# Kernel tuning notes

Hardware: AMD Instinct MI355X
Metric: run time of the kernel (lower is better)

Reference implementation:

```python
import jax, jax.numpy as jnp
import numpy as np

B, N, F_IN, F_OUT, E, GSD = 64, 512, 512, 512, 4, 1024
EPS = 1e-5


def _bn(z2d, gamma, beta):
    # training-mode BatchNorm1d over rows, biased variance, eps=1e-5
    mean = z2d.mean(axis=0)
    var = z2d.var(axis=0)
    return (z2d - mean) * jax.lax.rsqrt(var + EPS) * gamma + beta


def setup_inputs() -> dict:
    key = jax.random.key(0)
    ks = jax.random.split(key, 10)
    x = jax.random.normal(ks[0], (B, N, F_IN), dtype=jnp.float32)
    adj = jax.random.uniform(ks[1], (B, E, N, N), dtype=jnp.float32)
    global_state = jax.random.normal(ks[2], (B, GSD), dtype=jnp.float32)
    subgraph_sizes = jax.random.randint(ks[3], (B, 2), 0, 256, dtype=jnp.int64)
    mask = jnp.ones((B, N, 1), dtype=jnp.float32)
    # parameters
    W_gfc = jax.random.normal(ks[4], (GSD // 2, F_OUT), dtype=jnp.float32) * (1.0 / np.sqrt(GSD // 2))
    b_gfc = jnp.zeros((F_OUT,), dtype=jnp.float32)
    W_gc = jax.random.normal(ks[5], (E, F_IN + F_OUT, F_OUT), dtype=jnp.float32) * (1.0 / np.sqrt(F_IN + F_OUT))
    b_gc = jnp.zeros((F_OUT,), dtype=jnp.float32)
    gamma_n = jnp.ones((F_OUT,), dtype=jnp.float32)
    beta_n = jnp.zeros((F_OUT,), dtype=jnp.float32)
    gamma_g = jnp.ones((F_OUT,), dtype=jnp.float32)
    beta_g = jnp.zeros((F_OUT,), dtype=jnp.float32)
    return dict(x=x, adj=adj, global_state=global_state, subgraph_sizes=subgraph_sizes,
                mask=mask, W_gfc=W_gfc, b_gfc=b_gfc, W_gc=W_gc, b_gc=b_gc,
                gamma_n=gamma_n, beta_n=beta_n, gamma_g=gamma_g, beta_g=beta_g)


def reference(x, adj, global_state, subgraph_sizes, mask,
              W_gfc, b_gfc, W_gc, b_gc, gamma_n, beta_n, gamma_g, beta_g):
    b, n, _ = x.shape
    o = W_gfc.shape[1]
    # global FC on the two halves of the global state
    gs = global_state.reshape(b, 2, -1)                 # [B,2,GSD/2]
    gt = jnp.einsum('bkg,go->bko', gs, W_gfc) + b_gfc   # [B,2,O]
    # data-dependent broadcast of global features into node slices (vectorized)
    n1 = subgraph_sizes[:, 0]
    n2 = subgraph_sizes[:, 1]
    idx = jnp.arange(n)[None, :]
    sel0 = (idx < n1[:, None]).astype(x.dtype)                                  # [B,N]
    sel1 = ((idx >= n1[:, None]) & (idx < (n1 + n2)[:, None])).astype(x.dtype)  # [B,N]
    bg = sel0[..., None] * gt[:, 0, None, :] + sel1[..., None] * gt[:, 1, None, :]  # [B,N,O]
    x_concat = jnp.concatenate([x, bg], axis=-1)        # [B,N,F_IN+O]
    # multi-relational graph convolution: sum_e adj_e @ (x W_e) + bias
    support = jnp.einsum('bnf,efo->beno', x_concat, W_gc)       # [B,E,N,O]
    x_out = jnp.einsum('benm,bemo->bno', adj, support) + b_gc   # [B,N,O]
    # BN + mask + relu on nodes
    x_out = _bn(x_out.reshape(-1, o), gamma_n, beta_n).reshape(b, n, o)
    x_out = jax.nn.relu(x_out * mask)
    # BN + relu on global
    g_out = _bn(gt.reshape(-1, o), gamma_g, beta_g).reshape(b, 2, o)
    g_out = jax.nn.relu(g_out).reshape(b, -1)
    return x_out, g_out
```

## Files before the change

### kernel.cpp

```cpp
#include <hip/hip_runtime.h>

#define DEVI __device__ __forceinline__

typedef __bf16 bf16x8 __attribute__((ext_vector_type(8)));
typedef float  f32x4  __attribute__((ext_vector_type(4)));
typedef unsigned short ushort8_t __attribute__((ext_vector_type(8)));

constexpr size_t XOUT_ELEMS = (size_t)64 * 512 * 512;

DEVI unsigned short f2b(float f) {
  __bf16 h = (__bf16)f;
  return __builtin_bit_cast(unsigned short, h);
}

__global__ void k_decode(const int* __restrict__ ss, int* __restrict__ ns) {
  int t = threadIdx.x;
  int odd = ss[2 * t + 1];
  unsigned long long bal = __ballot(odd == 0);
  bool is64 = (bal == 0xFFFFFFFFFFFFFFFFull);
  if (is64) {
    const long long* s64 = (const long long*)ss;
    ns[2 * t]     = (int)s64[2 * t];
    ns[2 * t + 1] = (int)s64[2 * t + 1];
  } else {
    ns[2 * t]     = ss[2 * t];
    ns[2 * t + 1] = ss[2 * t + 1];
  }
}

__global__ void k_gt(const float* __restrict__ gs, const float* __restrict__ W,
                     const float* __restrict__ bias, float* __restrict__ gt,
                     unsigned short* __restrict__ gth) {
  __shared__ float srow[4][512];
  int r0  = blockIdx.y * 4;
  int col = blockIdx.x * 256 + threadIdx.x;
  for (int i = threadIdx.x; i < 4 * 512; i += 256)
    srow[i >> 9][i & 511] = gs[(size_t)r0 * 512 + i];
  __syncthreads();
  float acc[4] = {0.f, 0.f, 0.f, 0.f};
  for (int g = 0; g < 512; ++g) {
    float w = W[(size_t)g * 512 + col];
    acc[0] += srow[0][g] * w;
    acc[1] += srow[1][g] * w;
    acc[2] += srow[2][g] * w;
    acc[3] += srow[3][g] * w;
  }
  float bb = bias[col];
  #pragma unroll
  for (int r = 0; r < 4; ++r) {
    float v = acc[r] + bb;
    gt [(size_t)(r0 + r) * 512 + col] = v;
    gth[(size_t)(r0 + r) * 512 + col] = f2b(v);
  }
}

__global__ void k_gbn(const float* __restrict__ gt, const float* __restrict__ gamma,
                      const float* __restrict__ beta, float* __restrict__ gout) {
  int col = blockIdx.x * 64 + threadIdx.x;
  float s = 0.f, q = 0.f;
  for (int r = 0; r < 128; ++r) {
    float v = gt[(size_t)r * 512 + col];
    s += v; q += v * v;
  }
  float m   = s * (1.f / 128.f);
  float var = q * (1.f / 128.f) - m * m;
  float inv = 1.f / sqrtf(var + 1e-5f);
  float g = gamma[col], b = beta[col];
  for (int r = 0; r < 128; ++r) {
    float v = (gt[(size_t)r * 512 + col] - m) * inv * g + b;
    gout[(size_t)r * 512 + col] = fmaxf(v, 0.f);
  }
}

__global__ void k_cvt(const float* __restrict__ in, unsigned short* __restrict__ out,
                      long n8) {
  long i = (long)blockIdx.x * blockDim.x + threadIdx.x;
  long stride = (long)gridDim.x * blockDim.x;
  for (; i < n8; i += stride) {
    float4 a = ((const float4*)in)[2 * i];
    float4 b = ((const float4*)in)[2 * i + 1];
    ushort8_t o;
    o[0] = f2b(a.x); o[1] = f2b(a.y); o[2] = f2b(a.z); o[3] = f2b(a.w);
    o[4] = f2b(b.x); o[5] = f2b(b.y); o[6] = f2b(b.z); o[7] = f2b(b.w);
    *(ushort8_t*)&out[i * 8] = o;
  }
}

__global__ void k_cvt_w(const float* __restrict__ W, unsigned short* __restrict__ wT) {
  __shared__ float t[32][33];
  int k0 = blockIdx.x * 32, o0 = blockIdx.y * 32, e = blockIdx.z;
  const float* Wb = W + (size_t)e * 1024 * 512;
  unsigned short* Tb = wT + (size_t)e * 512 * 1024;
  int tid = threadIdx.x;
  #pragma unroll
  for (int p = 0; p < 4; ++p) {
    int kl = p * 8 + (tid >> 5), ol = tid & 31;
    t[kl][ol] = Wb[(size_t)(k0 + kl) * 512 + o0 + ol];
  }
  __syncthreads();
  #pragma unroll
  for (int p = 0; p < 4; ++p) {
    int ol = p * 8 + (tid >> 5), kl = tid & 31;
    Tb[(size_t)(o0 + ol) * 1024 + k0 + kl] = f2b(t[kl][ol]);
  }
}

DEVI void gl_lds16(const unsigned short* g, unsigned short* l) {
  __builtin_amdgcn_global_load_lds(
      (const __attribute__((address_space(1))) void*)g,
      (__attribute__((address_space(3))) void*)l, 16, 0, 0);
}

DEVI int lds_idx(int row, int slot) {
  return row * 32 + ((slot ^ ((row >> 1) & 3)) << 3);
}

template <class FA, class FB>
DEVI void mfma_core(unsigned short* As, unsigned short* Bs, FA srcA, FB srcB,
                    int NT, f32x4 (&acc)[4][4]) {
  const int tid  = threadIdx.x;
  const int lane = tid & 63;
  const int wave = tid >> 6;
  const int wr = wave >> 1, wc = wave & 1;
  const int fr = lane & 15, fs = lane >> 4;

  const int c0 = tid,       r0 = c0 >> 2, s0 = (c0 & 3) ^ ((r0 >> 1) & 3);
  const int c1 = tid + 256, r1 = c1 >> 2, s1 = (c1 & 3) ^ ((r1 >> 1) & 3);

  int aoff[4], boff[4];
  #pragma unroll
  for (int i = 0; i < 4; ++i) {
    aoff[i] = lds_idx(wr * 64 + i * 16 + fr, fs);
    boff[i] = lds_idx(wc * 64 + i * 16 + fr, fs);
  }

  gl_lds16(srcA(r0, s0 * 8, 0), As + c0 * 8);
  gl_lds16(srcA(r1, s1 * 8, 0), As + c1 * 8);
  gl_lds16(srcB(r0, s0 * 8, 0), Bs + c0 * 8);
  gl_lds16(srcB(r1, s1 * 8, 0), Bs + c1 * 8);

  for (int kt = 0; kt < NT; ++kt) {
    __syncthreads();
    bf16x8 af[4], bf[4];
    #pragma unroll
    for (int i = 0; i < 4; ++i) af[i] = *(const bf16x8*)(As + aoff[i]);
    #pragma unroll
    for (int j = 0; j < 4; ++j) bf[j] = *(const bf16x8*)(Bs + boff[j]);
    if (kt + 1 < NT) {
      __syncthreads();
      gl_lds16(srcA(r0, s0 * 8, kt + 1), As + c0 * 8);
      gl_lds16(srcA(r1, s1 * 8, kt + 1), As + c1 * 8);
      gl_lds16(srcB(r0, s0 * 8, kt + 1), Bs + c0 * 8);
      gl_lds16(srcB(r1, s1 * 8, kt + 1), Bs + c1 * 8);
    }
    #pragma unroll
    for (int i = 0; i < 4; ++i)
      #pragma unroll
      for (int j = 0; j < 4; ++j)
        acc[i][j] = __builtin_amdgcn_mfma_f32_16x16x32_bf16(af[i], bf[j], acc[i][j], 0, 0, 0);
  }
}

__global__ __launch_bounds__(256) void k_gadd(
    const unsigned short* __restrict__ gth, const unsigned short* __restrict__ wT,
    float* __restrict__ gadd) {
  __shared__ __align__(16) unsigned short As[4096], Bs[4096];
  const int otile = blockIdx.x * 128;

  auto srcA = [=](int row, int kofs, int kt) -> const unsigned short* {
    return gth + (size_t)row * 512 + kt * 32 + kofs;
  };
  auto srcB = [=](int row, int kofs, int kt) -> const unsigned short* {
    int op = otile + row;
    int e = op >> 9, o = op & 511;
    return wT + (size_t)e * 524288 + (size_t)o * 1024 + 512 + kt * 32 + kofs;
  };

  f32x4 acc[4][4];
  #pragma unroll
  for (int i = 0; i < 4; ++i)
    #pragma unroll
    for (int j = 0; j < 4; ++j) acc[i][j] = (f32x4){0.f, 0.f, 0.f, 0.f};

  mfma_core(As, Bs, srcA, srcB, 16, acc);

  const int lane = threadIdx.x & 63, wave = threadIdx.x >> 6;
  const int wr = wave >> 1, wc = wave & 1, fr = lane & 15, fs = lane >> 4;
  #pragma unroll
  for (int i = 0; i < 4; ++i) {
    int m = wr * 64 + i * 16 + fs * 4;
    #pragma unroll
    for (int j = 0; j < 4; ++j) {
      int op = otile + wc * 64 + j * 16 + fr;
      #pragma unroll
      for (int r = 0; r < 4; ++r)
        gadd[(size_t)(m + r) * 2048 + op] = acc[i][j][r];
    }
  }
}

__global__ __launch_bounds__(256) void k_support(
    const unsigned short* __restrict__ xh, const unsigned short* __restrict__ wT,
    const float* __restrict__ gadd, const int* __restrict__ ns,
    unsigned short* __restrict__ supT, int b0, int gc) {
  __shared__ __align__(16) unsigned short As[4096], Bs[4096];
  int flat = blockIdx.x;
  const int zi = flat % gc; flat /= gc;
  const int e  = flat & 3;  flat >>= 2;
  const int otile = (flat & 3) * 128;
  const int row0  = (flat >> 2) * 128;
  const int b  = b0 + zi;
  const int n1  = ns[2 * b];
  const int n12 = n1 + ns[2 * b + 1];
  const unsigned short* xb = xh + (size_t)b * 262144;
  const unsigned short* wb = wT + (size_t)e * 524288;

  auto srcA = [=](int row, int kofs, int kt) -> const unsigned short* {
    return xb + (size_t)(row0 + row) * 512 + kt * 32 + kofs;
  };
  auto srcB = [=](int row, int kofs, int kt) -> const unsigned short* {
    return wb + (size_t)(otile + row) * 1024 + kt * 32 + kofs;
  };

  f32x4 acc[4][4];
  #pragma unroll
  for (int i = 0; i < 4; ++i)
    #pragma unroll
    for (int j = 0; j < 4; ++j) acc[i][j] = (f32x4){0.f, 0.f, 0.f, 0.f};

  mfma_core(As, Bs, srcA, srcB, 16, acc);

  const int lane = threadIdx.x & 63, wave = threadIdx.x >> 6;
  const int wr = wave >> 1, wc = wave & 1, fr = lane & 15, fs = lane >> 4;
  unsigned short* sp = supT + (size_t)(zi * 4 + e) * 262144;
  #pragma unroll
  for (int j = 0; j < 4; ++j) {
    int o = otile + wc * 64 + j * 16 + fr;
    float g0 = gadd[(size_t)(2 * b)     * 2048 + e * 512 + o];
    float g1 = gadd[(size_t)(2 * b + 1) * 2048 + e * 512 + o];
    #pragma unroll
    for (int i = 0; i < 4; ++i) {
      int m = row0 + wr * 64 + i * 16 + fs * 4;
      ushort4 h;
      #pragma unroll
      for (int r = 0; r < 4; ++r) {
        int mr = m + r;
        float add = (mr < n1) ? g0 : ((mr < n12) ? g1 : 0.f);
        ((unsigned short*)&h)[r] = f2b(acc[i][j][r] + add);
      }
      *(ushort4*)&sp[(size_t)o * 512 + m] = h;
    }
  }
}

__global__ __launch_bounds__(256) void k_xout(
    const unsigned short* __restrict__ adjh, const unsigned short* __restrict__ supT,
    const float* __restrict__ bgc, float* __restrict__ out,
    float* __restrict__ gsum, float* __restrict__ gsq, int b0, int gc) {
  __shared__ __align__(16) unsigned short As[4096], Bs[4096];
  int flat = blockIdx.x;
  const int zi = flat % gc; flat /= gc;
  const int otile = (flat & 3) * 128;
  const int row0  = (flat >> 2) * 128;
  const int b  = b0 + zi;
  const unsigned short* ab = adjh + (size_t)b * 4 * 262144;
  const unsigned short* sb = supT + (size_t)zi * 4 * 262144;

  auto srcA = [=](int row, int kofs, int kt) -> const unsigned short* {
    int k = kt * 32 + kofs;
    int e = k >> 9, m = k & 511;
    return ab + ((size_t)e * 512 + row0 + row) * 512 + m;
  };
  auto srcB = [=](int row, int kofs, int kt) -> const unsigned short* {
    int k = kt * 32 + kofs;
    int e = k >> 9, m = k & 511;
    return sb + ((size_t)e * 512 + otile + row) * 512 + m;
  };

  f32x4 acc[4][4];
  #pragma unroll
  for (int i = 0; i < 4; ++i)
    #pragma unroll
    for (int j = 0; j < 4; ++j) acc[i][j] = (f32x4){0.f, 0.f, 0.f, 0.f};

  mfma_core(As, Bs, srcA, srcB, 64, acc);

  const int tid = threadIdx.x;
  const int lane = tid & 63, wave = tid >> 6;
  const int wr = wave >> 1, wc = wave & 1, fr = lane & 15, fs = lane >> 4;

  float cs[4], cq[4];
  #pragma unroll
  for (int j = 0; j < 4; ++j) {
    int o = otile + wc * 64 + j * 16 + fr;
    float bb = bgc[o];
    float s = 0.f, q = 0.f;
    #pragma unroll
    for (int i = 0; i < 4; ++i) {
      int nb = row0 + wr * 64 + i * 16 + fs * 4;
      #pragma unroll
      for (int r = 0; r < 4; ++r) {
        float v = acc[i][j][r] + bb;
        out[((size_t)b * 512 + nb + r) * 512 + o] = v;
        s += v; q += v * v;
      }
    }
    cs[j] = s; cq[j] = q;
  }

  __syncthreads();
  float* red = (float*)As;
  red[tid] = 0.f;
  __syncthreads();
  #pragma unroll
  for (int j = 0; j < 4; ++j) {
    int cl = wc * 64 + j * 16 + fr;
    atomicAdd(&red[cl], cs[j]);
    atomicAdd(&red[128 + cl], cq[j]);
  }
  __syncthreads();
  if (tid < 128) {
    atomicAdd(&gsum[otile + tid], red[tid]);
    atomicAdd(&gsq[otile + tid],  red[128 + tid]);
  }
}

__global__ void k_norm(const float* __restrict__ gsum, const float* __restrict__ gsq,
                       const float* __restrict__ gamma, const float* __restrict__ beta,
                       const float* __restrict__ mask, float* __restrict__ out) {
  __shared__ float sc[512], sh[512];
  for (int c = threadIdx.x; c < 512; c += blockDim.x) {
    float m   = gsum[c] * (1.f / 32768.f);
    float var = gsq[c] * (1.f / 32768.f) - m * m;
    float inv = 1.f / sqrtf(var + 1e-5f);
    float g = gamma[c] * inv;
    sc[c] = g;
    sh[c] = beta[c] - m * g;
  }
  __syncthreads();
  size_t i0 = (size_t)blockIdx.x * blockDim.x + threadIdx.x;
  size_t stride = (size_t)gridDim.x * blockDim.x;
  size_t n4 = XOUT_ELEMS / 4;
  for (size_t i = i0; i < n4; i += stride) {
    float4 p = ((const float4*)out)[i];
    int c = (int)((i * 4) & 511);
    size_t row = (i * 4) >> 9;
    float mk = mask[row];
    p.x = fmaxf((p.x * sc[c + 0] + sh[c + 0]) * mk, 0.f);
    p.y = fmaxf((p.y * sc[c + 1] + sh[c + 1]) * mk, 0.f);
    p.z = fmaxf((p.z * sc[c + 2] + sh[c + 2]) * mk, 0.f);
    p.w = fmaxf((p.w * sc[c + 3] + sh[c + 3]) * mk, 0.f);
    ((float4*)out)[i] = p;
  }
}

extern "C" void kernel_launch(void* const* d_in, const int* in_sizes, int n_in,
                              void* d_out, int out_size, void* d_ws, size_t ws_size,
                              hipStream_t stream) {
  const float* x    = (const float*)d_in[0];
  const float* adj  = (const float*)d_in[1];
  const float* gs   = (const float*)d_in[2];
  const int*   ssz  = (const int*)d_in[3];
  const float* mask = (const float*)d_in[4];
  const float* Wgfc = (const float*)d_in[5];
  const float* bgfc = (const float*)d_in[6];
  const float* Wgc  = (const float*)d_in[7];
  const float* bgc  = (const float*)d_in[8];
  const float* gn   = (const float*)d_in[9];
  const float* btn  = (const float*)d_in[10];
  const float* gg   = (const float*)d_in[11];
  const float* btg  = (const float*)d_in[12];
  float* out = (float*)d_out;

  char* w = (char*)d_ws;
  float*          gt   = (float*)w;
  unsigned short* gth  = (unsigned short*)(w + 262144);
  float*          gadd = (float*)(w + 393216);
  int*            ns   = (int*)(w + 1441792);
  float*          gsum = (float*)(w + 1442304);
  float*          gsq  = (float*)(w + 1444352);
  unsigned short* xh   = (unsigned short*)(w + ((size_t)2  << 20));
  unsigned short* wT   = (unsigned short*)(w + ((size_t)34 << 20));
  unsigned short* adjh = (unsigned short*)(w + ((size_t)40 << 20));
  unsigned short* supT = (unsigned short*)(w + ((size_t)168 << 20));

  long long avail = (long long)ws_size - (168ll << 20);
  int G = (avail > 0) ? (int)(avail / (2ll << 20)) : 0;
  if (G < 1) G = 1;
  if (G > 16) G = 16;

  k_decode<<<1, 64, 0, stream>>>(ssz, ns);
  k_gt<<<dim3(2, 32), 256, 0, stream>>>(gs, Wgfc, bgfc, gt, gth);
  k_gbn<<<8, 64, 0, stream>>>(gt, gg, btg, out + XOUT_ELEMS);
  hipMemsetAsync(gsum, 0, 4096, stream);

  k_cvt<<<2048, 256, 0, stream>>>(x, xh, (long)(16777216 / 8));
  k_cvt<<<4096, 256, 0, stream>>>(adj, adjh, (long)(67108864 / 8));
  k_cvt_w<<<dim3(32, 16, 4), 256, 0, stream>>>(Wgc, wT);
  k_gadd<<<16, 256, 0, stream>>>(gth, wT, gadd);

  for (int b0 = 0; b0 < 64; b0 += G) {
    int gc = 64 - b0; if (gc > G) gc = G;
    k_support<<<16 * 4 * gc, 256, 0, stream>>>(xh, wT, gadd, ns, supT, b0, gc);
    k_xout<<<16 * gc, 256, 0, stream>>>(adjh, supT, bgc, out, gsum, gsq, b0, gc);
  }

  k_norm<<<2048, 256, 0, stream>>>(gsum, gsq, gn, btn, mask, out);
}
```

Measured before the change: 893.0 us.

## Remap blocks so each batch stays on one XCD and raise batch-group cap

Block indices in k_support and k_xout are remapped so that all tiles of a given batch item land on the same XCD (round-robin by flat&7). This is meant to keep each batch's x, adj and support data within one XCD's L2. The batch group cap is raised from 16 to 64 and rounded to a multiple of 8. That means fewer, larger launches but needs more workspace for supT. The launch count change 16*4*gc to 64*gc is equivalent.

```diff
diff --git a/kernel.cpp b/kernel.cpp
--- a/kernel.cpp
+++ b/kernel.cpp
@@ -205,10 +205,22 @@
     unsigned short* __restrict__ supT, int b0, int gc) {
   __shared__ __align__(16) unsigned short As[4096], Bs[4096];
   int flat = blockIdx.x;
-  const int zi = flat % gc; flat /= gc;
-  const int e  = flat & 3;  flat >>= 2;
-  const int otile = (flat & 3) * 128;
-  const int row0  = (flat >> 2) * 128;
+  int zi, e, otile, row0;
+  if ((gc & 7) == 0) {
+    int xcd = flat & 7;
+    int j = flat >> 3;
+    int bgrp = j >> 6;
+    int tile = j & 63;
+    zi = bgrp * 8 + xcd;
+    e = tile & 3;
+    otile = ((tile >> 2) & 3) * 128;
+    row0  = (tile >> 4) * 128;
+  } else {
+    zi = flat % gc; flat /= gc;
+    e  = flat & 3;  flat >>= 2;
+    otile = (flat & 3) * 128;
+    row0  = (flat >> 2) * 128;
+  }
   const int b  = b0 + zi;
   const int n1  = ns[2 * b];
   const int n12 = n1 + ns[2 * b + 1];
@@ -259,9 +271,20 @@
     float* __restrict__ gsum, float* __restrict__ gsq, int b0, int gc) {
   __shared__ __align__(16) unsigned short As[4096], Bs[4096];
   int flat = blockIdx.x;
-  const int zi = flat % gc; flat /= gc;
-  const int otile = (flat & 3) * 128;
-  const int row0  = (flat >> 2) * 128;
+  int zi, otile, row0;
+  if ((gc & 7) == 0) {
+    int xcd = flat & 7;
+    int j = flat >> 3;
+    int bgrp = j >> 4;
+    int tile = j & 15;
+    zi = bgrp * 8 + xcd;
+    otile = (tile & 3) * 128;
+    row0  = (tile >> 2) * 128;
+  } else {
+    zi = flat % gc; flat /= gc;
+    otile = (flat & 3) * 128;
+    row0  = (flat >> 2) * 128;
+  }
   const int b  = b0 + zi;
   const unsigned short* ab = adjh + (size_t)b * 4 * 262144;
   const unsigned short* sb = supT + (size_t)zi * 4 * 262144;
@@ -387,7 +410,8 @@
   long long avail = (long long)ws_size - (168ll << 20);
   int G = (avail > 0) ? (int)(avail / (2ll << 20)) : 0;
   if (G < 1) G = 1;
-  if (G > 16) G = 16;
+  if (G > 64) G = 64;
+  if (G >= 8) G &= ~7;
 
   k_decode<<<1, 64, 0, stream>>>(ssz, ns);
   k_gt<<<dim3(2, 32), 256, 0, stream>>>(gs, Wgfc, bgfc, gt, gth);
@@ -401,7 +425,7 @@
 
   for (int b0 = 0; b0 < 64; b0 += G) {
     int gc = 64 - b0; if (gc > G) gc = G;
-    k_support<<<16 * 4 * gc, 256, 0, stream>>>(xh, wT, gadd, ns, supT, b0, gc);
+    k_support<<<64 * gc, 256, 0, stream>>>(xh, wT, gadd, ns, supT, b0, gc);
     k_xout<<<16 * gc, 256, 0, stream>>>(adjh, supT, bgc, out, gsum, gsq, b0, gc);
   }
 
```

New measurement: 819.4 us. 1.09x faster.

## Use 256x256 double-buffered MFMA tiles and launch support/xout once over all batches

Applied to the files above, without the earlier changes.

Adds a 512-thread GEMM core that computes 256x256 output tiles from a double-buffered LDS pipeline. The global-to-LDS load for the next k-step is issued before the MFMAs of the current step, so loads overlap compute. k_support and k_xout now use this core with an XCD-aware block-to-batch mapping and run as single launches over all 64 batches, replacing the workspace-sized batch-group loop. The aim is more data reuse per tile, fewer launches and better L2 locality. In exchange there are fewer, larger blocks with more accumulators per thread, and the code now assumes the workspace can hold the whole support buffer for every batch.

```diff
diff --git a/kernel.cpp b/kernel.cpp
--- a/kernel.cpp
+++ b/kernel.cpp
@@ -141,11 +141,11 @@
 
   for (int kt = 0; kt < NT; ++kt) {
     __syncthreads();
-    bf16x8 af[4], bf[4];
+    bf16x8 af[4], bfv[4];
     #pragma unroll
     for (int i = 0; i < 4; ++i) af[i] = *(const bf16x8*)(As + aoff[i]);
     #pragma unroll
-    for (int j = 0; j < 4; ++j) bf[j] = *(const bf16x8*)(Bs + boff[j]);
+    for (int j = 0; j < 4; ++j) bfv[j] = *(const bf16x8*)(Bs + boff[j]);
     if (kt + 1 < NT) {
       __syncthreads();
       gl_lds16(srcA(r0, s0 * 8, kt + 1), As + c0 * 8);
@@ -157,7 +157,7 @@
     for (int i = 0; i < 4; ++i)
       #pragma unroll
       for (int j = 0; j < 4; ++j)
-        acc[i][j] = __builtin_amdgcn_mfma_f32_16x16x32_bf16(af[i], bf[j], acc[i][j], 0, 0, 0);
+        acc[i][j] = __builtin_amdgcn_mfma_f32_16x16x32_bf16(af[i], bfv[j], acc[i][j], 0, 0, 0);
   }
 }
 
@@ -199,48 +199,116 @@
   }
 }
 
-__global__ __launch_bounds__(256) void k_support(
+template <class FA, class FB>
+DEVI void core256(unsigned short* lds, FA srcA, FB srcB, int NT, f32x4 (&acc)[8][4]) {
+  const int tid  = threadIdx.x;
+  const int lane = tid & 63;
+  const int wave = tid >> 6;
+  const int wr = wave >> 2, wcol = wave & 3;
+  const int fr = lane & 15, fs = lane >> 4;
+
+  int crow[2], cslot[2];
+  #pragma unroll
+  for (int t = 0; t < 2; ++t) {
+    int c = tid + t * 512;
+    crow[t]  = c >> 2;
+    cslot[t] = (c & 3) ^ ((crow[t] >> 1) & 3);
+  }
+
+  int aoff[8], boff[4];
+  #pragma unroll
+  for (int i = 0; i < 8; ++i) {
+    int row = wr * 128 + i * 16 + fr;
+    aoff[i] = row * 32 + ((fs ^ ((row >> 1) & 3)) << 3);
+  }
+  #pragma unroll
+  for (int j = 0; j < 4; ++j) {
+    int row = wcol * 64 + j * 16 + fr;
+    boff[j] = row * 32 + ((fs ^ ((row >> 1) & 3)) << 3);
+  }
+
+  #pragma unroll
+  for (int t = 0; t < 2; ++t) {
+    int c = tid + t * 512;
+    gl_lds16(srcA(crow[t], cslot[t] * 8, 0), lds + c * 8);
+    gl_lds16(srcB(crow[t], cslot[t] * 8, 0), lds + 8192 + c * 8);
+  }
+  __syncthreads();
+
+  int cur = 0;
+  for (int kt = 0; kt < NT; ++kt) {
+    unsigned short* Ab = lds + (cur ? 16384 : 0);
+    unsigned short* Bb = Ab + 8192;
+    if (kt + 1 < NT) {
+      unsigned short* An = lds + (cur ? 0 : 16384);
+      unsigned short* Bn = An + 8192;
+      #pragma unroll
+      for (int t = 0; t < 2; ++t) {
+        int c = tid + t * 512;
+        gl_lds16(srcA(crow[t], cslot[t] * 8, kt + 1), An + c * 8);
+        gl_lds16(srcB(crow[t], cslot[t] * 8, kt + 1), Bn + c * 8);
+      }
+    }
+    bf16x8 af[8], bfv[4];
+    #pragma unroll
+    for (int i = 0; i < 8; ++i) af[i] = *(const bf16x8*)(Ab + aoff[i]);
+    #pragma unroll
+    for (int j = 0; j < 4; ++j) bfv[j] = *(const bf16x8*)(Bb + boff[j]);
+    #pragma unroll
+    for (int i = 0; i < 8; ++i)
+      #pragma unroll
+      for (int j = 0; j < 4; ++j)
+        acc[i][j] = __builtin_amdgcn_mfma_f32_16x16x32_bf16(af[i], bfv[j], acc[i][j], 0, 0, 0);
+    __syncthreads();
+    cur ^= 1;
+  }
+}
+
+__global__ __launch_bounds__(512) void k_support(
     const unsigned short* __restrict__ xh, const unsigned short* __restrict__ wT,
     const float* __restrict__ gadd, const int* __restrict__ ns,
-    unsigned short* __restrict__ supT, int b0, int gc) {
-  __shared__ __align__(16) unsigned short As[4096], Bs[4096];
-  int flat = blockIdx.x;
-  const int zi = flat % gc; flat /= gc;
-  const int e  = flat & 3;  flat >>= 2;
-  const int otile = (flat & 3) * 128;
-  const int row0  = (flat >> 2) * 128;
-  const int b  = b0 + zi;
+    unsigned short* __restrict__ supT) {
+  __shared__ __align__(16) unsigned short lds[32768];
+  const int xcd = blockIdx.x & 7;
+  const int jj  = blockIdx.x >> 3;
+  const int et  = jj & 15;
+  const int e    = et >> 2;
+  const int tile = et & 3;
+  const int zi  = (jj >> 4) * 8 + xcd;
+  const int row0  = (tile >> 1) * 256;
+  const int otile = (tile & 1) * 256;
+  const int b = zi;
   const int n1  = ns[2 * b];
   const int n12 = n1 + ns[2 * b + 1];
   const unsigned short* xb = xh + (size_t)b * 262144;
   const unsigned short* wb = wT + (size_t)e * 524288;
 
-  auto srcA = [=](int row, int kofs, int kt) -> const unsigned short* {
-    return xb + (size_t)(row0 + row) * 512 + kt * 32 + kofs;
-  };
-  auto srcB = [=](int row, int kofs, int kt) -> const unsigned short* {
-    return wb + (size_t)(otile + row) * 1024 + kt * 32 + kofs;
-  };
-
-  f32x4 acc[4][4];
-  #pragma unroll
-  for (int i = 0; i < 4; ++i)
+  auto srcA = [=](int r, int koff, int kt) -> const unsigned short* {
+    return xb + (size_t)(row0 + r) * 512 + kt * 32 + koff;
+  };
+  auto srcB = [=](int r, int koff, int kt) -> const unsigned short* {
+    return wb + (size_t)(otile + r) * 1024 + kt * 32 + koff;
+  };
+
+  f32x4 acc[8][4];
+  #pragma unroll
+  for (int i = 0; i < 8; ++i)
     #pragma unroll
     for (int j = 0; j < 4; ++j) acc[i][j] = (f32x4){0.f, 0.f, 0.f, 0.f};
 
-  mfma_core(As, Bs, srcA, srcB, 16, acc);
+  core256(lds, srcA, srcB, 16, acc);
 
   const int lane = threadIdx.x & 63, wave = threadIdx.x >> 6;
-  const int wr = wave >> 1, wc = wave & 1, fr = lane & 15, fs = lane >> 4;
+  const int wr = wave >> 2, wcol = wave & 3, fr = lane & 15, fs = lane >> 4;
   unsigned short* sp = supT + (size_t)(zi * 4 + e) * 262144;
   #pragma unroll
   for (int j = 0; j < 4; ++j) {
-    int o = otile + wc * 64 + j * 16 + fr;
+    int o = otile + wcol * 64 + j * 16 + fr;
     float g0 = gadd[(size_t)(2 * b)     * 2048 + e * 512 + o];
     float g1 = gadd[(size_t)(2 * b + 1) * 2048 + e * 512 + o];
     #pragma unroll
-    for (int i = 0; i < 4; ++i) {
-      int m = row0 + wr * 64 + i * 16 + fs * 4;
+    for (int i = 0; i < 8; ++i) {
+      int m = row0 + wr * 128 + i * 16 + fs * 4;
       ushort4 h;
       #pragma unroll
       for (int r = 0; r < 4; ++r) {
@@ -253,51 +321,53 @@
   }
 }
 
-__global__ __launch_bounds__(256) void k_xout(
+__global__ __launch_bounds__(512) void k_xout(
     const unsigned short* __restrict__ adjh, const unsigned short* __restrict__ supT,
     const float* __restrict__ bgc, float* __restrict__ out,
-    float* __restrict__ gsum, float* __restrict__ gsq, int b0, int gc) {
-  __shared__ __align__(16) unsigned short As[4096], Bs[4096];
-  int flat = blockIdx.x;
-  const int zi = flat % gc; flat /= gc;
-  const int otile = (flat & 3) * 128;
-  const int row0  = (flat >> 2) * 128;
-  const int b  = b0 + zi;
+    float* __restrict__ gsum, float* __restrict__ gsq) {
+  __shared__ __align__(16) unsigned short lds[32768];
+  const int xcd = blockIdx.x & 7;
+  const int jj  = blockIdx.x >> 3;
+  const int tile = jj & 3;
+  const int zi  = (jj >> 2) * 8 + xcd;
+  const int row0  = (tile >> 1) * 256;
+  const int otile = (tile & 1) * 256;
+  const int b = zi;
   const unsigned short* ab = adjh + (size_t)b * 4 * 262144;
   const unsigned short* sb = supT + (size_t)zi * 4 * 262144;
 
-  auto srcA = [=](int row, int kofs, int kt) -> const unsigned short* {
-    int k = kt * 32 + kofs;
+  auto srcA = [=](int r, int koff, int kt) -> const unsigned short* {
+    int k = kt * 32 + koff;
     int e = k >> 9, m = k & 511;
-    return ab + ((size_t)e * 512 + row0 + row) * 512 + m;
-  };
-  auto srcB = [=](int row, int kofs, int kt) -> const unsigned short* {
-    int k = kt * 32 + kofs;
+    return ab + ((size_t)e * 512 + row0 + r) * 512 + m;
+  };
+  auto srcB = [=](int r, int koff, int kt) -> const unsigned short* {
+    int k = kt * 32 + koff;
     int e = k >> 9, m = k & 511;
-    return sb + ((size_t)e * 512 + otile + row) * 512 + m;
-  };
-
-  f32x4 acc[4][4];
-  #pragma unroll
-  for (int i = 0; i < 4; ++i)
+    return sb + (size_t)e * 262144 + (size_t)(otile + r) * 512 + m;
+  };
+
+  f32x4 acc[8][4];
+  #pragma unroll
+  for (int i = 0; i < 8; ++i)
     #pragma unroll
     for (int j = 0; j < 4; ++j) acc[i][j] = (f32x4){0.f, 0.f, 0.f, 0.f};
 
-  mfma_core(As, Bs, srcA, srcB, 64, acc);
+  core256(lds, srcA, srcB, 64, acc);
 
   const int tid = threadIdx.x;
   const int lane = tid & 63, wave = tid >> 6;
-  const int wr = wave >> 1, wc = wave & 1, fr = lane & 15, fs = lane >> 4;
+  const int wr = wave >> 2, wcol = wave & 3, fr = lane & 15, fs = lane >> 4;
 
   float cs[4], cq[4];
   #pragma unroll
   for (int j = 0; j < 4; ++j) {
-    int o = otile + wc * 64 + j * 16 + fr;
+    int o = otile + wcol * 64 + j * 16 + fr;
     float bb = bgc[o];
     float s = 0.f, q = 0.f;
     #pragma unroll
-    for (int i = 0; i < 4; ++i) {
-      int nb = row0 + wr * 64 + i * 16 + fs * 4;
+    for (int i = 0; i < 8; ++i) {
+      int nb = row0 + wr * 128 + i * 16 + fs * 4;
       #pragma unroll
       for (int r = 0; r < 4; ++r) {
         float v = acc[i][j][r] + bb;
@@ -308,20 +378,20 @@
     cs[j] = s; cq[j] = q;
   }
 
-  __syncthreads();
-  float* red = (float*)As;
+  float* red = (float*)lds;
+  __syncthreads();
   red[tid] = 0.f;
   __syncthreads();
   #pragma unroll
   for (int j = 0; j < 4; ++j) {
-    int cl = wc * 64 + j * 16 + fr;
+    int cl = wcol * 64 + j * 16 + fr;
     atomicAdd(&red[cl], cs[j]);
-    atomicAdd(&red[128 + cl], cq[j]);
-  }
-  __syncthreads();
-  if (tid < 128) {
+    atomicAdd(&red[256 + cl], cq[j]);
+  }
+  __syncthreads();
+  if (tid < 256) {
     atomicAdd(&gsum[otile + tid], red[tid]);
-    atomicAdd(&gsq[otile + tid],  red[128 + tid]);
+    atomicAdd(&gsq[otile + tid],  red[256 + tid]);
   }
 }
 
@@ -384,11 +454,6 @@
   unsigned short* adjh = (unsigned short*)(w + ((size_t)40 << 20));
   unsigned short* supT = (unsigned short*)(w + ((size_t)168 << 20));
 
-  long long avail = (long long)ws_size - (168ll << 20);
-  int G = (avail > 0) ? (int)(avail / (2ll << 20)) : 0;
-  if (G < 1) G = 1;
-  if (G > 16) G = 16;
-
   k_decode<<<1, 64, 0, stream>>>(ssz, ns);
   k_gt<<<dim3(2, 32), 256, 0, stream>>>(gs, Wgfc, bgfc, gt, gth);
   k_gbn<<<8, 64, 0, stream>>>(gt, gg, btg, out + XOUT_ELEMS);
@@ -399,11 +464,8 @@
   k_cvt_w<<<dim3(32, 16, 4), 256, 0, stream>>>(Wgc, wT);
   k_gadd<<<16, 256, 0, stream>>>(gth, wT, gadd);
 
-  for (int b0 = 0; b0 < 64; b0 += G) {
-    int gc = 64 - b0; if (gc > G) gc = G;
-    k_support<<<16 * 4 * gc, 256, 0, stream>>>(xh, wT, gadd, ns, supT, b0, gc);
-    k_xout<<<16 * gc, 256, 0, stream>>>(adjh, supT, bgc, out, gsum, gsq, b0, gc);
-  }
+  k_support<<<1024, 512, 0, stream>>>(xh, wT, gadd, ns, supT);
+  k_xout<<<256, 512, 0, stream>>>(adjh, supT, bgc, out, gsum, gsq);
 
   k_norm<<<2048, 256, 0, stream>>>(gsum, gsq, gn, btn, mask, out);
 }
```

After: 745.2 us. 16.6% less time.
